# Performance work log

Measured on AMD Instinct MI355X. Metric: run time of the kernel, lower is better.

Reference implementation:

```python
import jax, jax.numpy as jnp
import numpy as np

MIN_SIZE = 25.0      # remove_small_boxes threshold (init default)
IOU_THRESH = 0.3     # nms iou_threshold (init default)
MAX_DET = 100        # rcnn_detections_per_image (init default)
IMG = 1024.0         # synthetic image size for box generation


def setup_inputs() -> dict:
    key = jax.random.key(0)
    k1, k2, k3 = jax.random.split(key, 3)
    B, N = 16, 4096
    # valid xyxy boxes inside a 1024x1024 image
    cxcy = jax.random.uniform(k1, (B, N, 2), minval=0.0, maxval=IMG)
    wh = jax.random.uniform(k2, (B, N, 2), minval=1.0, maxval=300.0)
    boxes = jnp.concatenate([cxcy - wh / 2, cxcy + wh / 2], axis=-1)
    boxes = jnp.clip(boxes, 0.0, IMG)
    scores = jax.random.uniform(k3, (B, N))
    return {"boxes": boxes, "scores": scores}


def _pairwise_iou(b):
    # b: [N,4] xyxy -> iou: [N,N]
    area = (b[:, 2] - b[:, 0]) * (b[:, 3] - b[:, 1])
    lt = jnp.maximum(b[:, None, :2], b[None, :, :2])
    rb = jnp.minimum(b[:, None, 2:], b[None, :, 2:])
    wh = jnp.clip(rb - lt, 0.0)
    inter = wh[..., 0] * wh[..., 1]
    return inter / (area[:, None] + area[None, :] - inter + 1e-9)


def _per_image(boxes, scores):
    # boxes [N,4], scores [N] -> (out_boxes [K,4], valid [K])
    N = boxes.shape[0]
    # remove_small_boxes: width and height >= min_size
    valid = ((boxes[:, 2] - boxes[:, 0]) >= MIN_SIZE) & ((boxes[:, 3] - boxes[:, 1]) >= MIN_SIZE)
    s = jnp.where(valid, scores, -jnp.inf)
    order = jnp.argsort(-s)          # score-descending, invalid boxes last
    b = boxes[order]
    v = valid[order]
    iou = _pairwise_iou(b)           # [N,N] dominant intermediate
    idx = jnp.arange(N)

    def body(i, keep):
        # greedy NMS: box i (if kept) suppresses lower-scored overlapping boxes
        sup = (iou[i] > IOU_THRESH) & keep[i] & (idx > i)
        return keep & ~sup

    keep = jax.lax.fori_loop(0, N, body, v)
    # first MAX_DET kept boxes in score order (fixed-shape top-k truncation)
    sel = jnp.argsort(jnp.where(keep, idx, N))[:MAX_DET]
    valid_out = jnp.take(keep, sel)
    out_boxes = jnp.where(valid_out[:, None], b[sel], 0.0)
    return out_boxes, valid_out


def reference(boxes, scores):
    # boxes [B,N,4], scores [B,N] -> [B,K,5] rows (image_idx, x1,y1,x2,y2);
    # padded rows have image_idx = -1 (fixed-shape analogue of the ragged concat)
    out_boxes, valid = jax.vmap(_per_image)(boxes, scores)
    B = boxes.shape[0]
    img_idx = jnp.where(valid, jnp.arange(B, dtype=boxes.dtype)[:, None], -1.0)
    return jnp.concatenate([img_idx[..., None], out_boxes], axis=-1)
```

## Files before the change

kernel.cpp:

```cpp
#include <hip/hip_runtime.h>
#include <math.h>

#define N_BOX 4096
#define B_IMG 16
#define MAXDET 100
#define MINSZ 25.0f
#define IOUT 0.3f
#define NBUCK 1024

__device__ __forceinline__ float iou_f(float ax1, float ay1, float ax2, float ay2, float aarea,
                                       float bx1, float by1, float bx2, float by2, float barea) {
#pragma clang fp contract(off)
    float lx = fmaxf(ax1, bx1);
    float ly = fmaxf(ay1, by1);
    float rx = fminf(ax2, bx2);
    float ry = fminf(ay2, by2);
    float wx = fmaxf(rx - lx, 0.0f);
    float wy = fmaxf(ry - ly, 0.0f);
    float inter = wx * wy;
    float denom = ((aarea + barea) - inter) + 1e-9f;
    return inter / denom;
}

__global__ __launch_bounds__(256) void fused_kernel(
        const float4* __restrict__ boxes, const float* __restrict__ scores,
        float* __restrict__ out) {
    __shared__ __align__(16) unsigned long long bkey[N_BOX];
    __shared__ unsigned short sinv[N_BOX];
    __shared__ int cnt[NBUCK];
    __shared__ int start[NBUCK];
    __shared__ int chunkInv[64];
    __shared__ int chunkPre[64];
    __shared__ int scratch[256];
    __shared__ int wsum[4];
    __shared__ int nvalidS;
    __shared__ __align__(16) float4 kbox[384];
    __shared__ int scnt[4];

    int b = blockIdx.x;
    int t = threadIdx.x;
    int w = t >> 6, l = t & 63;
    const float4* bb = boxes + (size_t)b * N_BOX;
    const float* ss = scores + (size_t)b * N_BOX;

    for (int q = t; q < NBUCK; q += 256) cnt[q] = 0;
    __syncthreads();

    unsigned long long key[16];
    int buck[16];
    unsigned char ipre[16];
    unsigned vmask = 0;
#pragma unroll
    for (int p = 0; p < 16; ++p) {
        int i = w * 64 + 256 * p + l;
        float4 bx = bb[i];
        float sc = ss[i];
        bool valid = ((bx.z - bx.x) >= MINSZ) && ((bx.w - bx.y) >= MINSZ);
        float k = valid ? sc : -INFINITY;
        unsigned u = __float_as_uint(k);
        u = (u & 0x80000000u) ? ~u : (u | 0x80000000u);
        key[p] = ((unsigned long long)u << 12) | (unsigned long long)(N_BOX - 1 - i);
        unsigned long long im = __ballot(!valid);
        ipre[p] = (unsigned char)__popcll(im & ((1ull << l) - 1ull));
        if (l == 0) chunkInv[w + 4 * p] = __popcll(im);
        if (valid) {
            vmask |= (1u << p);
            int bk = (int)(sc * 1024.0f);
            bk = bk < 0 ? 0 : (bk > NBUCK - 1 ? NBUCK - 1 : bk);
            buck[p] = bk;
            atomicAdd(&cnt[bk], 1);
        }
    }
    __syncthreads();

    if (t < 64) {
        int v = chunkInv[t];
        int x = v;
        for (int off = 1; off < 64; off <<= 1) {
            int y = __shfl_up(x, off);
            if (l >= off) x += y;
        }
        chunkPre[t] = x - v;
        if (t == 63) nvalidS = N_BOX - x;
    }
    __syncthreads();

    int S = 0;
#pragma unroll
    for (int q = 0; q < 4; ++q) S += cnt[t * 4 + q];
    scratch[255 - t] = S;
    __syncthreads();
    int xv = scratch[t];
    int incl = xv;
    for (int off = 1; off < 64; off <<= 1) {
        int y = __shfl_up(incl, off);
        if (l >= off) incl += y;
    }
    if (l == 63) wsum[w] = incl;
    __syncthreads();
    int woff = 0;
    for (int q = 0; q < w; ++q) woff += wsum[q];
    int excl = woff + incl - xv;
    __syncthreads();
    scratch[t] = excl;
    __syncthreads();
    int T = scratch[255 - t];
    int running = T;
#pragma unroll
    for (int q = 3; q >= 0; --q) {
        start[t * 4 + q] = running;
        running += cnt[t * 4 + q];
    }
    __syncthreads();

#pragma unroll
    for (int p = 0; p < 16; ++p) {
        if (vmask & (1u << p)) {
            int ps = atomicAdd(&start[buck[p]], 1);
            bkey[ps] = key[p];
        }
    }
    __syncthreads();

    int nvalid = nvalidS;
#pragma unroll
    for (int p = 0; p < 16; ++p) {
        int i = w * 64 + 256 * p + l;
        int r;
        unsigned vbit = (vmask >> p) & 1u;
        if (vbit) {
            int bk = buck[p];
            int end = start[bk];
            int beg = end - cnt[bk];
            unsigned long long mk = key[p];
            r = beg;
            for (int q = beg; q < end; ++q)
                r += (bkey[q] > mk) ? 1 : 0;
        } else {
            r = nvalid + chunkPre[w + 4 * p] + (int)ipre[p];
        }
        sinv[r] = (unsigned short)(i | (vbit << 15));
    }
    __syncthreads();

    int kept = 0;
    for (int g = 0; g < 16; ++g) {
        int c = g * 4 + w;
        unsigned short e = sinv[c * 64 + l];
        float4 bx = bb[e & 0xFFFu];
        float x1 = bx.x, y1 = bx.y, x2 = bx.z, y2 = bx.w;
        float ar;
        {
#pragma clang fp contract(off)
            ar = (x2 - x1) * (y2 - y1);
        }
        bool alive = (e >> 15) != 0;
        int K0 = kept;
        for (int q = 0; q < K0; ++q) {
            float4 kb = kbox[q];
            float kar;
            {
#pragma clang fp contract(off)
                kar = (kb.z - kb.x) * (kb.w - kb.y);
            }
            float v = iou_f(kb.x, kb.y, kb.z, kb.w, kar, x1, y1, x2, y2, ar);
            if (v > IOUT) alive = false;
        }
        for (int s = 0; s < 4; ++s) {
            if (w == s) {
                int Kcur = K0;
                for (int ss2 = 0; ss2 < s; ++ss2) Kcur += scnt[ss2];
                int cnt2 = 0;
                if (Kcur < MAXDET) {
                    for (int q = K0; q < Kcur; ++q) {
                        float4 kb = kbox[q];
                        float kar;
                        {
#pragma clang fp contract(off)
                            kar = (kb.z - kb.x) * (kb.w - kb.y);
                        }
                        float v = iou_f(kb.x, kb.y, kb.z, kb.w, kar, x1, y1, x2, y2, ar);
                        if (v > IOUT) alive = false;
                    }
                    unsigned long long m = __ballot(alive);
                    unsigned long long mm = m;
                    while (mm) {
                        int i = __ffsll(mm) - 1;
                        float bx1 = __shfl(x1, i), by1 = __shfl(y1, i);
                        float bx2 = __shfl(x2, i), by2 = __shfl(y2, i);
                        float ba  = __shfl(ar, i);
                        float v = iou_f(bx1, by1, bx2, by2, ba, x1, y1, x2, y2, ar);
                        bool sup = (l > i) && (v > IOUT) && ((m >> l) & 1ull);
                        unsigned long long sm = __ballot(sup);
                        m &= ~sm;
                        mm &= ~(1ull << i);
                        mm &= m;
                    }
                    cnt2 = __popcll(m);
                    int pos = Kcur + __popcll(m & ((1ull << l) - 1ull));
                    if ((m >> l) & 1ull) kbox[pos] = make_float4(x1, y1, x2, y2);
                }
                if (l == 0) scnt[s] = cnt2;
            }
            __syncthreads();
        }
        kept = K0 + scnt[0] + scnt[1] + scnt[2] + scnt[3];
        __syncthreads();
        if (kept >= MAXDET) break;
    }

    int tot = kept < MAXDET ? kept : MAXDET;
    float* ob = out + (size_t)b * MAXDET * 5;
    for (int r = t; r < MAXDET; r += 256) {
        float* row = ob + r * 5;
        if (r < tot) {
            float4 kb = kbox[r];
            row[0] = (float)b;
            row[1] = kb.x; row[2] = kb.y; row[3] = kb.z; row[4] = kb.w;
        } else {
            row[0] = -1.0f;
            row[1] = 0.0f; row[2] = 0.0f; row[3] = 0.0f; row[4] = 0.0f;
        }
    }
}

extern "C" void kernel_launch(void* const* d_in, const int* in_sizes, int n_in,
                              void* d_out, int out_size, void* d_ws, size_t ws_size,
                              hipStream_t stream) {
    const float4* boxes = (const float4*)d_in[0];
    const float* scores = (const float*)d_in[1];
    float* out = (float*)d_out;
    (void)d_ws; (void)ws_size;

    fused_kernel<<<B_IMG, 256, 0, stream>>>(boxes, scores, out);
}
```

Measured before the change: 103.1 us.

## Use 8 waves per block, replace IoU division with threshold compare, cache kept areas

Doubles the block to 512 threads (8 waves), so each thread handles 8 boxes instead of 16 in the sort phase and each NMS round covers 512 candidates. The IoU division is replaced by a double-precision multiply-compare against a constant chosen to match the float `> 0.3` test. Areas of kept boxes are stored in shared memory instead of being recomputed. The wider round adds a longer serial wave-by-wave scan with more barriers per round, and the double-precision compare could cost more than the division it replaces.

```diff
diff --git a/kernel.cpp b/kernel.cpp
--- a/kernel.cpp
+++ b/kernel.cpp
@@ -5,11 +5,12 @@
 #define B_IMG 16
 #define MAXDET 100
 #define MINSZ 25.0f
-#define IOUT 0.3f
 #define NBUCK 1024
-
-__device__ __forceinline__ float iou_f(float ax1, float ay1, float ax2, float ay2, float aarea,
-                                       float bx1, float by1, float bx2, float by2, float barea) {
+#define NW 8
+#define NT 512
+
+__device__ __forceinline__ bool sup_test(float ax1, float ay1, float ax2, float ay2, float aarea,
+                                         float bx1, float by1, float bx2, float by2, float barea) {
 #pragma clang fp contract(off)
     float lx = fmaxf(ax1, bx1);
     float ly = fmaxf(ay1, by1);
@@ -19,10 +20,11 @@
     float wy = fmaxf(ry - ly, 0.0f);
     float inter = wx * wy;
     float denom = ((aarea + barea) - inter) + 1e-9f;
-    return inter / denom;
+    const double M = 0x1.333335p-2;
+    return (double)inter > M * (double)denom;
 }
 
-__global__ __launch_bounds__(256) void fused_kernel(
+__global__ __launch_bounds__(NT) void fused_kernel(
         const float4* __restrict__ boxes, const float* __restrict__ scores,
         float* __restrict__ out) {
     __shared__ __align__(16) unsigned long long bkey[N_BOX];
@@ -31,11 +33,12 @@
     __shared__ int start[NBUCK];
     __shared__ int chunkInv[64];
     __shared__ int chunkPre[64];
-    __shared__ int scratch[256];
-    __shared__ int wsum[4];
+    __shared__ int scratch[NT];
+    __shared__ int wsum[NW];
     __shared__ int nvalidS;
-    __shared__ __align__(16) float4 kbox[384];
-    __shared__ int scnt[4];
+    __shared__ __align__(16) float4 kbox[192];
+    __shared__ float kar[192];
+    __shared__ int scnt[NW];
 
     int b = blockIdx.x;
     int t = threadIdx.x;
@@ -43,16 +46,16 @@
     const float4* bb = boxes + (size_t)b * N_BOX;
     const float* ss = scores + (size_t)b * N_BOX;
 
-    for (int q = t; q < NBUCK; q += 256) cnt[q] = 0;
-    __syncthreads();
-
-    unsigned long long key[16];
-    int buck[16];
-    unsigned char ipre[16];
+    for (int q = t; q < NBUCK; q += NT) cnt[q] = 0;
+    __syncthreads();
+
+    unsigned long long key[8];
+    int buck[8];
+    unsigned char ipre[8];
     unsigned vmask = 0;
 #pragma unroll
-    for (int p = 0; p < 16; ++p) {
-        int i = w * 64 + 256 * p + l;
+    for (int p = 0; p < 8; ++p) {
+        int i = w * 64 + NT * p + l;
         float4 bx = bb[i];
         float sc = ss[i];
         bool valid = ((bx.z - bx.x) >= MINSZ) && ((bx.w - bx.y) >= MINSZ);
@@ -62,7 +65,7 @@
         key[p] = ((unsigned long long)u << 12) | (unsigned long long)(N_BOX - 1 - i);
         unsigned long long im = __ballot(!valid);
         ipre[p] = (unsigned char)__popcll(im & ((1ull << l) - 1ull));
-        if (l == 0) chunkInv[w + 4 * p] = __popcll(im);
+        if (l == 0) chunkInv[w + NW * p] = __popcll(im);
         if (valid) {
             vmask |= (1u << p);
             int bk = (int)(sc * 1024.0f);
@@ -85,10 +88,8 @@
     }
     __syncthreads();
 
-    int S = 0;
-#pragma unroll
-    for (int q = 0; q < 4; ++q) S += cnt[t * 4 + q];
-    scratch[255 - t] = S;
+    int S = cnt[2 * t] + cnt[2 * t + 1];
+    scratch[NT - 1 - t] = S;
     __syncthreads();
     int xv = scratch[t];
     int incl = xv;
@@ -104,17 +105,13 @@
     __syncthreads();
     scratch[t] = excl;
     __syncthreads();
-    int T = scratch[255 - t];
-    int running = T;
+    int T = scratch[NT - 1 - t];
+    start[2 * t + 1] = T;
+    start[2 * t] = T + cnt[2 * t + 1];
+    __syncthreads();
+
 #pragma unroll
-    for (int q = 3; q >= 0; --q) {
-        start[t * 4 + q] = running;
-        running += cnt[t * 4 + q];
-    }
-    __syncthreads();
-
-#pragma unroll
-    for (int p = 0; p < 16; ++p) {
+    for (int p = 0; p < 8; ++p) {
         if (vmask & (1u << p)) {
             int ps = atomicAdd(&start[buck[p]], 1);
             bkey[ps] = key[p];
@@ -124,8 +121,8 @@
 
     int nvalid = nvalidS;
 #pragma unroll
-    for (int p = 0; p < 16; ++p) {
-        int i = w * 64 + 256 * p + l;
+    for (int p = 0; p < 8; ++p) {
+        int i = w * 64 + NT * p + l;
         int r;
         unsigned vbit = (vmask >> p) & 1u;
         if (vbit) {
@@ -137,15 +134,15 @@
             for (int q = beg; q < end; ++q)
                 r += (bkey[q] > mk) ? 1 : 0;
         } else {
-            r = nvalid + chunkPre[w + 4 * p] + (int)ipre[p];
+            r = nvalid + chunkPre[w + NW * p] + (int)ipre[p];
         }
         sinv[r] = (unsigned short)(i | (vbit << 15));
     }
     __syncthreads();
 
     int kept = 0;
-    for (int g = 0; g < 16; ++g) {
-        int c = g * 4 + w;
+    for (int g = 0; g < 8; ++g) {
+        int c = g * NW + w;
         unsigned short e = sinv[c * 64 + l];
         float4 bx = bb[e & 0xFFFu];
         float x1 = bx.x, y1 = bx.y, x2 = bx.z, y2 = bx.w;
@@ -158,15 +155,10 @@
         int K0 = kept;
         for (int q = 0; q < K0; ++q) {
             float4 kb = kbox[q];
-            float kar;
-            {
-#pragma clang fp contract(off)
-                kar = (kb.z - kb.x) * (kb.w - kb.y);
-            }
-            float v = iou_f(kb.x, kb.y, kb.z, kb.w, kar, x1, y1, x2, y2, ar);
-            if (v > IOUT) alive = false;
-        }
-        for (int s = 0; s < 4; ++s) {
+            if (sup_test(kb.x, kb.y, kb.z, kb.w, kar[q], x1, y1, x2, y2, ar))
+                alive = false;
+        }
+        for (int s = 0; s < NW; ++s) {
             if (w == s) {
                 int Kcur = K0;
                 for (int ss2 = 0; ss2 < s; ++ss2) Kcur += scnt[ss2];
@@ -174,13 +166,8 @@
                 if (Kcur < MAXDET) {
                     for (int q = K0; q < Kcur; ++q) {
                         float4 kb = kbox[q];
-                        float kar;
-                        {
-#pragma clang fp contract(off)
-                            kar = (kb.z - kb.x) * (kb.w - kb.y);
-                        }
-                        float v = iou_f(kb.x, kb.y, kb.z, kb.w, kar, x1, y1, x2, y2, ar);
-                        if (v > IOUT) alive = false;
+                        if (sup_test(kb.x, kb.y, kb.z, kb.w, kar[q], x1, y1, x2, y2, ar))
+                            alive = false;
                     }
                     unsigned long long m = __ballot(alive);
                     unsigned long long mm = m;
@@ -189,8 +176,8 @@
                         float bx1 = __shfl(x1, i), by1 = __shfl(y1, i);
                         float bx2 = __shfl(x2, i), by2 = __shfl(y2, i);
                         float ba  = __shfl(ar, i);
-                        float v = iou_f(bx1, by1, bx2, by2, ba, x1, y1, x2, y2, ar);
-                        bool sup = (l > i) && (v > IOUT) && ((m >> l) & 1ull);
+                        bool sup = (l > i) && ((m >> l) & 1ull) &&
+                                   sup_test(bx1, by1, bx2, by2, ba, x1, y1, x2, y2, ar);
                         unsigned long long sm = __ballot(sup);
                         m &= ~sm;
                         mm &= ~(1ull << i);
@@ -198,20 +185,25 @@
                     }
                     cnt2 = __popcll(m);
                     int pos = Kcur + __popcll(m & ((1ull << l) - 1ull));
-                    if ((m >> l) & 1ull) kbox[pos] = make_float4(x1, y1, x2, y2);
+                    if ((m >> l) & 1ull) {
+                        kbox[pos] = make_float4(x1, y1, x2, y2);
+                        kar[pos] = ar;
+                    }
                 }
                 if (l == 0) scnt[s] = cnt2;
             }
             __syncthreads();
         }
-        kept = K0 + scnt[0] + scnt[1] + scnt[2] + scnt[3];
+        int knew = K0;
+        for (int q = 0; q < NW; ++q) knew += scnt[q];
+        kept = knew;
         __syncthreads();
         if (kept >= MAXDET) break;
     }
 
     int tot = kept < MAXDET ? kept : MAXDET;
     float* ob = out + (size_t)b * MAXDET * 5;
-    for (int r = t; r < MAXDET; r += 256) {
+    for (int r = t; r < MAXDET; r += NT) {
         float* row = ob + r * 5;
         if (r < tot) {
             float4 kb = kbox[r];
@@ -232,5 +224,5 @@
     float* out = (float*)d_out;
     (void)d_ws; (void)ws_size;
 
-    fused_kernel<<<B_IMG, 256, 0, stream>>>(boxes, scores, out);
+    fused_kernel<<<B_IMG, NT, 0, stream>>>(boxes, scores, out);
 }
```

Result: faster. 91.54 us (-11.2%).
